# Kernel tuning notes

Hardware: AMD Instinct MI355X
Metric: run time of the kernel (lower is better)

The kernel has to match this reference:

```python
import jax, jax.numpy as jnp
import numpy as np

N, S, D = 16, 32, 256      # batch, seq_len, hidden_size
B = 4                      # sample_size (Monte-Carlo beams)
CH = 4 * D                 # cell_hidden_dim = 4*hidden (hard-coded in __init__)
EPS = 1e-20


def _ln(x, g, b):
    m = x.mean(-1, keepdims=True)
    v = ((x - m) ** 2).mean(-1, keepdims=True)
    return (x - m) / jnp.sqrt(v + 1e-5) * g + b


def _masked_softmax(logits, mask):
    p = jax.nn.softmax(logits, axis=-1)
    p = p * mask + EPS
    return p / p.sum(-1, keepdims=True)


def _cell(l, r, w1, b1, w2, b2, ln2_g, ln2_b):
    # TreeLSTM-style fused cell: Linear -> GELU -> Linear -> gates -> LayerNorm
    cat = jnp.concatenate([l, r], axis=-1)                  # (NB, s, 2D)
    inter = jax.nn.gelu(cat @ w1 + b1, approximate=False)   # (NB, s, 4D)
    contents = (inter @ w2 + b2).reshape(*l.shape[:-1], 4, D)
    gates = jax.nn.sigmoid(contents[..., 0:3, :])
    f1, f2, ig = gates[..., 0, :], gates[..., 1, :], gates[..., 2, :]
    parent = contents[..., 3, :]
    return _ln(f1 * l + f2 * r + ig * parent, ln2_g, ln2_b)


def _select(old_h, new_h, mask, accu, dec_W, dec_b, key):
    NB, Sc, Dd = new_h.shape
    old_l, old_r = old_h[:, :-1], old_h[:, 1:]
    nh = new_h * mask[:, :, None]
    pad = jnp.zeros((NB, 1, Dd), nh.dtype)
    l1 = jnp.concatenate([pad, nh[:, :-1]], axis=1)
    l2 = jnp.concatenate([pad, l1[:, :-1]], axis=1)
    r1 = jnp.concatenate([nh[:, 1:], pad], axis=1)
    r2 = jnp.concatenate([r1[:, 1:], pad], axis=1)
    win = jnp.concatenate([l2, l1, nh, r1, r2], axis=-1)    # (NB, Sc, 5D)
    logits = (win @ dec_W + dec_b)[..., 0] / np.sqrt(5 * Dd)
    # straight-through Gumbel softmax (temperature = 1)
    u = jax.random.uniform(key, logits.shape, logits.dtype)
    g = -jnp.log(-jnp.log(u + EPS) + EPS)
    y_soft = _masked_softmax(logits + g, mask)
    y_hard = jax.nn.one_hot(jnp.argmax(y_soft, axis=-1), Sc, dtype=y_soft.dtype)
    sel = jax.lax.stop_gradient(y_hard - y_soft) + y_soft
    soft_scores = jnp.sum(sel * _masked_softmax(logits, mask), axis=1)
    accu = accu + jnp.log(soft_scores + EPS)
    cs = jnp.cumsum(sel, axis=1)
    left = (1.0 - cs)[:, :, None]
    right = (cs - sel)[:, :, None]
    merged = sel[:, :, None] * new_h + left * old_l + right * old_r
    return merged, accu


def setup_inputs() -> dict:
    key = jax.random.key(0)
    ks = jax.random.split(key, 6)
    f32 = jnp.float32
    return {
        "x": jax.random.normal(ks[0], (N, S, D), f32),
        "input_mask": jnp.ones((N, S), f32),
        "word_W": jax.random.normal(ks[1], (D, D), f32) / np.sqrt(D),
        "word_b": jnp.zeros((D,), f32),
        "ln_g": jnp.ones((D,), f32),
        "ln_b": jnp.zeros((D,), f32),
        "w1": jax.random.normal(ks[2], (2 * D, CH), f32) / np.sqrt(2 * D),
        "b1": jnp.zeros((CH,), f32),
        "w2": jax.random.normal(ks[3], (CH, 4 * D), f32) / np.sqrt(CH),
        "b2": jnp.zeros((4 * D,), f32),
        "ln2_g": jnp.ones((D,), f32),
        "ln2_b": jnp.zeros((D,), f32),
        "dec_W": jax.random.normal(ks[4], (5 * D, 1), f32) / np.sqrt(5 * D),
        "dec_b": jnp.zeros((1,), f32),
    }


def reference(x, input_mask, word_W, word_b, ln_g, ln_b, w1, b1, w2, b2,
              ln2_g, ln2_b, dec_W, dec_b):
    state = _ln(x @ word_W + word_b, ln_g, ln_b)                 # (N, S, D)
    state = jnp.repeat(state[:, None], B, axis=1).reshape(N * B, S, D)
    lmask = jnp.repeat(input_mask[:, None], B, axis=1).reshape(N * B, S)
    accu = jnp.zeros((N * B,), state.dtype)
    base = jax.random.key(1234)
    # sequential tree-building recurrence; sequence axis shrinks by 1 each step
    for i in range(S - 1):
        l, r = state[:, :-1], state[:, 1:]
        new_state = _cell(l, r, w1, b1, w2, b2, ln2_g, ln2_b)
        if i < S - 2:
            new_state, new_accu = _select(state, new_state, lmask[:, i + 1:],
                                          accu, dec_W, dec_b,
                                          jax.random.fold_in(base, i))
        else:
            new_accu = accu
        done = lmask[:, i + 1]
        state = done[:, None, None] * new_state + (1.0 - done[:, None, None]) * state[:, :-1]
        accu = done * new_accu + (1.0 - done) * accu
    h = state[:, 0].reshape(N, B, D)
    scores = jax.nn.softmax(accu.reshape(N, B, 1), axis=1)
    return jnp.sum(scores * h, axis=1)                            # (N, D)
```

## Files before the change

kernel.cpp:

```cpp
#include <hip/hip_runtime.h>
#include <cstdint>
#include <cstddef>

namespace {
constexpr int kP0 = 31;
constexpr int kM0 = 496;
}

__device__ float g_state[2][64 * 32 * 256];
__device__ float g_nh[2][64 * kP0 * 256];
__device__ float g_s5[2][64 * kP0 * 5];
__device__ float g_nh0[kM0 * 256];
__device__ float g_s50[kM0 * 5];
__device__ float g_inter0[(size_t)kM0 * 1024];
__device__ float g_cont0[(size_t)kM0 * 1024];
__device__ float g_p1[4][128 * 1024];
__device__ float g_p2[4][128 * 1024];
__device__ float g_accu[64];
__device__ int g_slots[2][128];

__device__ __forceinline__ void tf2x32(uint32_t k0, uint32_t k1, uint32_t x0,
                                       uint32_t x1, uint32_t& o0, uint32_t& o1) {
  uint32_t ks2 = k0 ^ k1 ^ 0x1BD11BDAu;
  x0 += k0; x1 += k1;
#define TF_ROT(v, r) (((v) << (r)) | ((v) >> (32 - (r))))
#define TF_RD(r) { x0 += x1; x1 = TF_ROT(x1, r); x1 ^= x0; }
  TF_RD(13) TF_RD(15) TF_RD(26) TF_RD(6)   x0 += k1;  x1 += ks2 + 1u;
  TF_RD(17) TF_RD(29) TF_RD(16) TF_RD(24)  x0 += ks2; x1 += k0 + 2u;
  TF_RD(13) TF_RD(15) TF_RD(26) TF_RD(6)   x0 += k0;  x1 += k1 + 3u;
  TF_RD(17) TF_RD(29) TF_RD(16) TF_RD(24)  x0 += k1;  x1 += ks2 + 4u;
  TF_RD(13) TF_RD(15) TF_RD(26) TF_RD(6)   x0 += ks2; x1 += k0 + 5u;
  o0 = x0; o1 = x1;
#undef TF_RD
#undef TF_ROT
}

__device__ __forceinline__ float blockSum256(float v, float* red4, int tid) {
#pragma unroll
  for (int o = 32; o > 0; o >>= 1) v += __shfl_down(v, o, 64);
  __syncthreads();
  if ((tid & 63) == 0) red4[tid >> 6] = v;
  __syncthreads();
  return red4[0] + red4[1] + red4[2] + red4[3];
}
__device__ __forceinline__ float waveMax64(float v) {
#pragma unroll
  for (int o = 32; o > 0; o >>= 1) v = fmaxf(v, __shfl_xor(v, o, 64));
  return v;
}
__device__ __forceinline__ float waveSum64(float v) {
#pragma unroll
  for (int o = 32; o > 0; o >>= 1) v += __shfl_xor(v, o, 64);
  return v;
}
__device__ __forceinline__ float geluf(float v) {
  return 0.5f * v * (1.0f + erff(v * 0.70710678118654752440f));
}

__global__ __launch_bounds__(256) void k_embed(const float* __restrict__ x,
                                               const float* __restrict__ wW,
                                               const float* __restrict__ wb,
                                               const float* __restrict__ lng,
                                               const float* __restrict__ lnb) {
  int row = blockIdx.x;
  int d = threadIdx.x;
  __shared__ float xs[256];
  __shared__ float red4[4];
  xs[d] = x[row * 256 + d];
  __syncthreads();
  float acc = wb[d];
  for (int k = 0; k < 256; ++k) acc = fmaf(xs[k], wW[k * 256 + d], acc);
  float mean = blockSum256(acc, red4, d) * (1.0f / 256.0f);
  float cen = acc - mean;
  float var = blockSum256(cen * cen, red4, d) * (1.0f / 256.0f);
  float o = cen / sqrtf(var + 1e-5f) * lng[d] + lnb[d];
  int n = row >> 5, s = row & 31;
#pragma unroll
  for (int bb = 0; bb < 4; ++bb)
    g_state[0][((n * 4 + bb) * 32 + s) * 256 + d] = o;
  if (row == 0 && d < 64) g_accu[d] = 0.0f;
}


__global__ __launch_bounds__(256) void k_g1s(const float* __restrict__ w1,
                                             const float* __restrict__ b1) {
  __shared__ float As[64][17];
  __shared__ float Ws[64][68];
  const int tid = threadIdx.x;
  const int colB = blockIdx.x * 64;
  const int rowB = blockIdx.y * 16;
  const int row = tid >> 4, cg = tid & 15;
  const int ar = tid >> 4, ak = (tid & 15) * 4;
  const float* Ab;
  {
    int m = rowB + ar;
    int n = m / 31, j = m - n * 31;
    Ab = g_state[0] + (n * 4) * 8192 + j * 256;
  }
  float4 aR = *(const float4*)&Ab[ak];
  float4 wR[4];
#pragma unroll
  for (int q = 0; q < 4; ++q) {
    int f = tid + q * 256; int kk = f >> 4, c4 = f & 15;
    wR[q] = *(const float4*)&w1[(size_t)kk * 1024 + colB + c4 * 4];
  }
  float acc[4] = {};
  for (int c = 0; c < 8; ++c) {
    As[ak + 0][ar] = aR.x; As[ak + 1][ar] = aR.y;
    As[ak + 2][ar] = aR.z; As[ak + 3][ar] = aR.w;
#pragma unroll
    for (int q = 0; q < 4; ++q) {
      int f = tid + q * 256; int kk = f >> 4, c4 = f & 15;
      *(float4*)&Ws[kk][c4 * 4] = wR[q];
    }
    __syncthreads();
    if (c < 7) {
      int kb = (c + 1) * 64;
      aR = *(const float4*)&Ab[kb + ak];
#pragma unroll
      for (int q = 0; q < 4; ++q) {
        int f = tid + q * 256; int kk = f >> 4, c4 = f & 15;
        wR[q] = *(const float4*)&w1[(size_t)(kb + kk) * 1024 + colB + c4 * 4];
      }
    }
#pragma unroll
    for (int kk = 0; kk < 64; ++kk) {
      float a = As[kk][row];
      float4 w = *(const float4*)&Ws[kk][cg * 4];
      acc[0] = fmaf(a, w.x, acc[0]); acc[1] = fmaf(a, w.y, acc[1]);
      acc[2] = fmaf(a, w.z, acc[2]); acc[3] = fmaf(a, w.w, acc[3]);
    }
    __syncthreads();
  }
  int m = rowB + row;
  int col = colB + cg * 4;
  float4 bb = *(const float4*)&b1[col];
  float4 o;
  o.x = geluf(acc[0] + bb.x); o.y = geluf(acc[1] + bb.y);
  o.z = geluf(acc[2] + bb.z); o.w = geluf(acc[3] + bb.w);
  *(float4*)&g_inter0[(size_t)m * 1024 + col] = o;
}

__global__ __launch_bounds__(256) void k_g2s(const float* __restrict__ w2) {
  __shared__ float As[64][17];
  __shared__ float Ws[64][68];
  const int tid = threadIdx.x;
  const int colB = blockIdx.x * 64;
  const int rowB = blockIdx.y * 16;
  const int row = tid >> 4, cg = tid & 15;
  const int ar = tid >> 4, ak = (tid & 15) * 4;
  const float* Ab = g_inter0 + (size_t)(rowB + ar) * 1024;
  float4 aR = *(const float4*)&Ab[ak];
  float4 wR[4];
#pragma unroll
  for (int q = 0; q < 4; ++q) {
    int f = tid + q * 256; int kk = f >> 4, c4 = f & 15;
    wR[q] = *(const float4*)&w2[(size_t)kk * 1024 + colB + c4 * 4];
  }
  float acc[4] = {};
  for (int c = 0; c < 16; ++c) {
    As[ak + 0][ar] = aR.x; As[ak + 1][ar] = aR.y;
    As[ak + 2][ar] = aR.z; As[ak + 3][ar] = aR.w;
#pragma unroll
    for (int q = 0; q < 4; ++q) {
      int f = tid + q * 256; int kk = f >> 4, c4 = f & 15;
      *(float4*)&Ws[kk][c4 * 4] = wR[q];
    }
    __syncthreads();
    if (c < 15) {
      int kb = (c + 1) * 64;
      aR = *(const float4*)&Ab[kb + ak];
#pragma unroll
      for (int q = 0; q < 4; ++q) {
        int f = tid + q * 256; int kk = f >> 4, c4 = f & 15;
        wR[q] = *(const float4*)&w2[(size_t)(kb + kk) * 1024 + colB + c4 * 4];
      }
    }
#pragma unroll
    for (int kk = 0; kk < 64; ++kk) {
      float a = As[kk][row];
      float4 w = *(const float4*)&Ws[kk][cg * 4];
      acc[0] = fmaf(a, w.x, acc[0]); acc[1] = fmaf(a, w.y, acc[1]);
      acc[2] = fmaf(a, w.z, acc[2]); acc[3] = fmaf(a, w.w, acc[3]);
    }
    __syncthreads();
  }
  int m = rowB + row;
  int col = colB + cg * 4;
  float4 o = {acc[0], acc[1], acc[2], acc[3]};
  *(float4*)&g_cont0[(size_t)m * 1024 + col] = o;
}

__device__ __forceinline__ float4 g2t_loadA(int grow, int kpos, const float* __restrict__ b1) {
  size_t g = (size_t)grow * 1024 + kpos;
  float4 p0 = *(const float4*)&g_p1[0][g];
  float4 p1 = *(const float4*)&g_p1[1][g];
  float4 p2 = *(const float4*)&g_p1[2][g];
  float4 p3 = *(const float4*)&g_p1[3][g];
  float4 bb = *(const float4*)&b1[kpos];
  float4 r;
  r.x = geluf(p0.x + p1.x + p2.x + p3.x + bb.x);
  r.y = geluf(p0.y + p1.y + p2.y + p3.y + bb.y);
  r.z = geluf(p0.z + p1.z + p2.z + p3.z + bb.z);
  r.w = geluf(p0.w + p1.w + p2.w + p3.w + bb.w);
  return r;
}

__global__ __launch_bounds__(256) void k_g2t(const float* __restrict__ w2,
                                             const float* __restrict__ b1) {
  __shared__ float As[64][17];
  __shared__ float Ws[64][68];
  const int tid = threadIdx.x;
  const int colB = blockIdx.x * 64;
  const int rowB = blockIdx.y * 16;
  const int Ks = blockIdx.z;
  const int kb0 = Ks * 256;
  const int row = tid >> 4, cg = tid & 15;
  const int ar = tid >> 4, ak = (tid & 15) * 4;
  const int grow = rowB + ar;
  float4 aR = g2t_loadA(grow, kb0 + ak, b1);
  float4 wR[4];
#pragma unroll
  for (int q = 0; q < 4; ++q) {
    int f = tid + q * 256; int kk = f >> 4, c4 = f & 15;
    wR[q] = *(const float4*)&w2[(size_t)(kb0 + kk) * 1024 + colB + c4 * 4];
  }
  float acc[4] = {};
  for (int c = 0; c < 4; ++c) {
    As[ak + 0][ar] = aR.x; As[ak + 1][ar] = aR.y;
    As[ak + 2][ar] = aR.z; As[ak + 3][ar] = aR.w;
#pragma unroll
    for (int q = 0; q < 4; ++q) {
      int f = tid + q * 256; int kk = f >> 4, c4 = f & 15;
      *(float4*)&Ws[kk][c4 * 4] = wR[q];
    }
    __syncthreads();
    if (c < 3) {
      int kb = kb0 + (c + 1) * 64;
      aR = g2t_loadA(grow, kb + ak, b1);
#pragma unroll
      for (int q = 0; q < 4; ++q) {
        int f = tid + q * 256; int kk = f >> 4, c4 = f & 15;
        wR[q] = *(const float4*)&w2[(size_t)(kb + kk) * 1024 + colB + c4 * 4];
      }
    }
#pragma unroll
    for (int kk = 0; kk < 64; ++kk) {
      float a = As[kk][row];
      float4 w = *(const float4*)&Ws[kk][cg * 4];
      acc[0] = fmaf(a, w.x, acc[0]); acc[1] = fmaf(a, w.y, acc[1]);
      acc[2] = fmaf(a, w.z, acc[2]); acc[3] = fmaf(a, w.w, acc[3]);
    }
    __syncthreads();
  }
  int col = colB + cg * 4;
  float4 o = {acc[0], acc[1], acc[2], acc[3]};
  *(float4*)&g_p2[Ks][(rowB + row) * 1024 + col] = o;
}

__global__ __launch_bounds__(256) void k_cellfull(const float* __restrict__ imask,
                                                  const float* __restrict__ ln2g,
                                                  const float* __restrict__ ln2b,
                                                  const float* __restrict__ decW,
                                                  const float* __restrict__ b2) {
  int m = blockIdx.x;
  int d = threadIdx.x;
  int n = m / 31, j = m - n * 31;
  const float* st = g_state[0] + (n * 4) * 8192;
  const float* crow = g_cont0 + (size_t)m * 1024;
  float c0 = crow[d] + b2[d];
  float c1 = crow[256 + d] + b2[256 + d];
  float c2 = crow[512 + d] + b2[512 + d];
  float c3 = crow[768 + d] + b2[768 + d];
  float l = st[j * 256 + d];
  float r = st[(j + 1) * 256 + d];
  float f1 = 1.0f / (1.0f + expf(-c0));
  float f2 = 1.0f / (1.0f + expf(-c1));
  float ig = 1.0f / (1.0f + expf(-c2));
  float pre = f1 * l + f2 * r + ig * c3;
  __shared__ float red4[4];
  __shared__ float w5[4][5];
  float mean = blockSum256(pre, red4, d) * (1.0f / 256.0f);
  float cen = pre - mean;
  float var = blockSum256(cen * cen, red4, d) * (1.0f / 256.0f);
  float nh = cen / sqrtf(var + 1e-5f) * ln2g[d] + ln2b[d];
  g_nh0[m * 256 + d] = nh;
  float mv = imask[n * 32 + 1 + j];
  float nhm = nh * mv;
  float pv[5];
#pragma unroll
  for (int t = 0; t < 5; ++t) pv[t] = nhm * decW[t * 256 + d];
#pragma unroll
  for (int t = 0; t < 5; ++t)
#pragma unroll
    for (int o = 32; o > 0; o >>= 1) pv[t] += __shfl_down(pv[t], o, 64);
  __syncthreads();
  if ((d & 63) == 0) {
#pragma unroll
    for (int t = 0; t < 5; ++t) w5[d >> 6][t] = pv[t];
  }
  __syncthreads();
  if (d < 5) g_s50[m * 5 + d] = w5[0][d] + w5[1][d] + w5[2][d] + w5[3][d];
}

__global__ __launch_bounds__(256) void k_cm(
    const float* __restrict__ imask, const float* __restrict__ decW,
    const float* __restrict__ decb, const float* __restrict__ b2,
    const float* __restrict__ ln2g, const float* __restrict__ ln2b,
    const float* __restrict__ w1, int i, int last) {
  const int b = blockIdx.x, grp = blockIdx.y;
  const int tid = threadIdx.x, st = tid, lane = tid & 63, wv = tid >> 6;
  const int Sc = 31 - i;
  const int buf = i & 1;
  const int n32 = (b >> 2) * 32;
  __shared__ float sh_nhf[2][256];
  __shared__ float sh_s5f[2][5];
  __shared__ float sA[3][256];
  __shared__ float red4[4];
  __shared__ float w5s[4][5];
  __shared__ int sh_k;
  __shared__ float sh_sv;
  int slot0 = -1, slot1 = -1;
  if (i > 0) { slot0 = g_slots[buf][2 * b]; slot1 = g_slots[buf][2 * b + 1]; }
  const float* s5Src = (i == 0) ? (g_s50 + (b >> 2) * kP0 * 5) : (g_s5[buf] + b * kP0 * 5);
  const float* nhSrcG = (i == 0) ? (g_nh0 + (size_t)(b >> 2) * kP0 * 256)
                                 : (g_nh[buf] + (size_t)b * kP0 * 256);
  const float* stOld = g_state[buf] + b * 8192;
  float* stNew = g_state[(i + 1) & 1] + b * 8192;
  float* nhDst = g_nh[(i + 1) & 1] + (size_t)b * kP0 * 256;
  float* s5Dst = g_s5[(i + 1) & 1] + b * kP0 * 5;
  float done = imask[n32 + i + 1];

  if (i > 0) {
#pragma unroll 1
    for (int s = 0; s < 2; ++s) {
      int j = (s == 0) ? slot0 : slot1;
      if (j < 0) continue;
      int sr = 2 * b + s;
      float c[4];
#pragma unroll
      for (int q = 0; q < 4; ++q) {
        int g = sr * 1024 + q * 256 + st;
        float v = ((g_p2[0][g] + g_p2[1][g]) + g_p2[2][g]) + g_p2[3][g];
        c[q] = v + b2[q * 256 + st];
      }
      float l = stOld[j * 256 + st];
      float r = stOld[(j + 1) * 256 + st];
      float f1 = 1.0f / (1.0f + expf(-c[0]));
      float f2 = 1.0f / (1.0f + expf(-c[1]));
      float ig = 1.0f / (1.0f + expf(-c[2]));
      float pre = f1 * l + f2 * r + ig * c[3];
      float mean = blockSum256(pre, red4, st) * (1.0f / 256.0f);
      float cen = pre - mean;
      float var = blockSum256(cen * cen, red4, st) * (1.0f / 256.0f);
      float nh = cen / sqrtf(var + 1e-5f) * ln2g[st] + ln2b[st];
      sh_nhf[s][st] = nh;
      float mv = imask[n32 + i + 1 + j];
      float nhm = nh * mv;
      float pv[5];
#pragma unroll
      for (int t = 0; t < 5; ++t) pv[t] = nhm * decW[t * 256 + st];
#pragma unroll
      for (int t = 0; t < 5; ++t) {
        float v = pv[t];
#pragma unroll
        for (int o = 32; o > 0; o >>= 1) v += __shfl_down(v, o, 64);
        pv[t] = v;
      }
      __syncthreads();
      if (lane == 0) {
#pragma unroll
        for (int t = 0; t < 5; ++t) w5s[wv][t] = pv[t];
      }
      __syncthreads();
      if (st < 5) sh_s5f[s][st] = w5s[0][st] + w5s[1][st] + w5s[2][st] + w5s[3][st];
    }
  }
  __syncthreads();

  if (!last && tid < 64) {
    int j = lane;
    bool act = j < Sc;
    float mv = 0.f, lg = 0.f;
    if (act) {
      mv = imask[n32 + i + 1 + j];
      float t5 = decb[0];
      if (j >= 2) {
        int rw = j - 2;
        t5 += (i > 0 && rw == slot0) ? sh_s5f[0][0] : (i > 0 && rw == slot1) ? sh_s5f[1][0] : s5Src[rw * 5 + 0];
      }
      if (j >= 1) {
        int rw = j - 1;
        t5 += (i > 0 && rw == slot0) ? sh_s5f[0][1] : (i > 0 && rw == slot1) ? sh_s5f[1][1] : s5Src[rw * 5 + 1];
      }
      {
        int rw = j;
        t5 += (i > 0 && rw == slot0) ? sh_s5f[0][2] : (i > 0 && rw == slot1) ? sh_s5f[1][2] : s5Src[rw * 5 + 2];
      }
      if (j + 1 < Sc) {
        int rw = j + 1;
        t5 += (i > 0 && rw == slot0) ? sh_s5f[0][3] : (i > 0 && rw == slot1) ? sh_s5f[1][3] : s5Src[rw * 5 + 3];
      }
      if (j + 2 < Sc) {
        int rw = j + 2;
        t5 += (i > 0 && rw == slot0) ? sh_s5f[0][4] : (i > 0 && rw == slot1) ? sh_s5f[1][4] : s5Src[rw * 5 + 4];
      }
      lg = t5 / 35.77708763999664f;
    }
    uint32_t fk0, fk1, o0, o1;
    tf2x32(0u, 1234u, 0u, (uint32_t)i, fk0, fk1);
    uint32_t idx = (uint32_t)(b * Sc + j);
    tf2x32(fk0, fk1, 0u, idx, o0, o1);
    uint32_t bits = o0 ^ o1;
    float u = __uint_as_float((bits >> 9) | 0x3f800000u) - 1.0f;
    float gum = -logf(-logf(u + 1e-20f) + 1e-20f);
    float z = lg + gum;
    float zm = waveMax64(act ? z : -3.0e38f);
    float e = act ? expf(z - zm) : 0.f;
    float p = e / waveSum64(e);
    float y = act ? (p * mv + 1e-20f) : 0.f;
    float ys = y / waveSum64(y);
    float av = act ? ys : -1.f;
    int ai = j;
#pragma unroll
    for (int o = 32; o > 0; o >>= 1) {
      float ov = __shfl_xor(av, o, 64);
      int oi = __shfl_xor(ai, o, 64);
      if (ov > av || (ov == av && oi < ai)) { av = ov; ai = oi; }
    }
    float lm = waveMax64(act ? lg : -3.0e38f);
    float e2 = act ? expf(lg - lm) : 0.f;
    float p2 = e2 / waveSum64(e2);
    float y2 = act ? (p2 * mv + 1e-20f) : 0.f;
    float ps = y2 / waveSum64(y2);
    float ysk = __shfl(ys, ai, 64);
    float psk = __shfl(ps, ai, 64);
    float sv = (1.0f - ysk) + ysk;
    if (j == 0) {
      sh_k = ai;
      sh_sv = sv;
      if (grp == 0) {
        g_accu[b] += done * logf(sv * psk + 1e-20f);
        int s0 = -1, s1 = -1;
        if (done != 0.0f) {
          if (ai >= 1) s0 = ai - 1;
          if (ai <= Sc - 2) s1 = ai;
        }
        g_slots[(i + 1) & 1][2 * b] = s0;
        g_slots[(i + 1) & 1][2 * b + 1] = s1;
      }
    }
  }
  __syncthreads();

  if (last) {
    if (grp == 0 && wv == 0) {
      float4 ol = *(const float4*)&stOld[lane * 4];
      float4 nh4;
      if (slot0 == 0) nh4 = *(const float4*)&sh_nhf[0][lane * 4];
      else if (slot1 == 0) nh4 = *(const float4*)&sh_nhf[1][lane * 4];
      else nh4 = *(const float4*)&nhSrcG[lane * 4];
      float4 o4;
      o4.x = done * nh4.x + (1.0f - done) * ol.x;
      o4.y = done * nh4.y + (1.0f - done) * ol.y;
      o4.z = done * nh4.z + (1.0f - done) * ol.z;
      o4.w = done * nh4.w + (1.0f - done) * ol.w;
      *(float4*)&stNew[lane * 4] = o4;
    }
    return;
  }

  int k = sh_k;
  float sv = sh_sv;
  {
    int jrow = grp * 4 + wv;
    if (jrow < Sc) {
      float4 ol = *(const float4*)&stOld[jrow * 256 + lane * 4];
      float4 ov4;
      if (done != 0.0f) {
        float4 mg;
        if (jrow < k) {
          mg = ol;
        } else if (jrow == k) {
          float4 nh4 = (i > 0 && k == slot0) ? *(const float4*)&sh_nhf[0][lane * 4]
                     : (i > 0 && k == slot1) ? *(const float4*)&sh_nhf[1][lane * 4]
                     : *(const float4*)&nhSrcG[k * 256 + lane * 4];
          mg.x = sv * nh4.x + (1.0f - sv) * ol.x;
          mg.y = sv * nh4.y + (1.0f - sv) * ol.y;
          mg.z = sv * nh4.z + (1.0f - sv) * ol.z;
          mg.w = sv * nh4.w + (1.0f - sv) * ol.w;
        } else {
          float4 orr = *(const float4*)&stOld[(jrow + 1) * 256 + lane * 4];
          mg.x = (1.0f - sv) * ol.x + sv * orr.x;
          mg.y = (1.0f - sv) * ol.y + sv * orr.y;
          mg.z = (1.0f - sv) * ol.z + sv * orr.z;
          mg.w = (1.0f - sv) * ol.w + sv * orr.w;
        }
        ov4.x = done * mg.x + (1.0f - done) * ol.x;
        ov4.y = done * mg.y + (1.0f - done) * ol.y;
        ov4.z = done * mg.z + (1.0f - done) * ol.z;
        ov4.w = done * mg.w + (1.0f - done) * ol.w;
      } else {
        ov4 = ol;
      }
      *(float4*)&stNew[jrow * 256 + lane * 4] = ov4;
      if (jrow < Sc - 1) {
        int src = (done != 0.0f && jrow > k) ? jrow + 1 : jrow;
        float4 nv = (i > 0 && src == slot0) ? *(const float4*)&sh_nhf[0][lane * 4]
                  : (i > 0 && src == slot1) ? *(const float4*)&sh_nhf[1][lane * 4]
                  : *(const float4*)&nhSrcG[src * 256 + lane * 4];
        *(float4*)&nhDst[jrow * 256 + lane * 4] = nv;
        float mv2 = imask[n32 + i + 2 + jrow];
        float pv[5];
#pragma unroll
        for (int t = 0; t < 5; ++t) {
          const float* dw = decW + t * 256 + lane * 4;
          pv[t] = (nv.x * dw[0] + nv.y * dw[1] + nv.z * dw[2] + nv.w * dw[3]) * mv2;
        }
#pragma unroll
        for (int t = 0; t < 5; ++t) {
          float v = pv[t];
#pragma unroll
          for (int o = 32; o > 0; o >>= 1) v += __shfl_down(v, o, 64);
          pv[t] = v;
        }
        if (lane == 0) {
#pragma unroll
          for (int t = 0; t < 5; ++t) s5Dst[jrow * 5 + t] = pv[t];
        }
      }
    }
  }

  if (done != 0.0f) {
    __syncthreads();
    {
      int d = st;
      float nhKv = (i > 0 && k == slot0) ? sh_nhf[0][d]
                 : (i > 0 && k == slot1) ? sh_nhf[1][d]
                 : nhSrcG[k * 256 + d];
#pragma unroll
      for (int t = 0; t < 3; ++t) {
        int r = k - 1 + t;
        if (r < 0 || r > Sc - 1) continue;
        float ol = stOld[r * 256 + d];
        float mg;
        if (r < k) mg = ol;
        else if (r == k) mg = sv * nhKv + (1.0f - sv) * ol;
        else mg = (1.0f - sv) * ol + sv * stOld[(r + 1) * 256 + d];
        sA[t][d] = done * mg + (1.0f - done) * ol;
      }
    }
    __syncthreads();
    const int my = grp >> 2;
    const int Ks = grp & 3;
    const int has = (my == 0) ? (k >= 1) : (k <= Sc - 2);
    const int kb0 = Ks * 128;
    const float* A = (my == 0) ? ((Ks < 2) ? sA[0] : sA[1])
                               : ((Ks < 2) ? sA[1] : sA[2]);
    const int koff = (Ks < 2) ? kb0 : (kb0 - 256);
    const int col = st * 4;
    float a0 = 0.f, a1 = 0.f, a2 = 0.f, a3 = 0.f;
    for (int kk = 0; kk < 128; ++kk) {
      float4 w = *(const float4*)&w1[(size_t)(kb0 + kk) * 1024 + col];
      float av = A[koff + kk];
      a0 = fmaf(av, w.x, a0); a1 = fmaf(av, w.y, a1);
      a2 = fmaf(av, w.z, a2); a3 = fmaf(av, w.w, a3);
    }
    if (has) {
      float4 o = {a0, a1, a2, a3};
      *(float4*)&g_p1[Ks][(2 * b + my) * 1024 + col] = o;
    }
  }
}

__global__ __launch_bounds__(256) void k_final(float* __restrict__ out) {
  int n = blockIdx.x, d = threadIdx.x;
  float a0 = g_accu[n * 4 + 0], a1 = g_accu[n * 4 + 1];
  float a2 = g_accu[n * 4 + 2], a3 = g_accu[n * 4 + 3];
  float mx = fmaxf(fmaxf(a0, a1), fmaxf(a2, a3));
  float e0 = expf(a0 - mx), e1 = expf(a1 - mx), e2 = expf(a2 - mx), e3 = expf(a3 - mx);
  float ssum = e0 + e1 + e2 + e3;
  const float* st1 = g_state[1];
  float h0 = st1[(n * 4 + 0) * 8192 + d];
  float h1 = st1[(n * 4 + 1) * 8192 + d];
  float h2 = st1[(n * 4 + 2) * 8192 + d];
  float h3 = st1[(n * 4 + 3) * 8192 + d];
  out[n * 256 + d] = (e0 / ssum) * h0 + (e1 / ssum) * h1 + (e2 / ssum) * h2 + (e3 / ssum) * h3;
}

extern "C" void kernel_launch(void* const* d_in, const int* in_sizes, int n_in,
                              void* d_out, int out_size, void* d_ws, size_t ws_size,
                              hipStream_t stream) {
  (void)in_sizes; (void)n_in; (void)d_ws; (void)ws_size; (void)out_size;
  const float* x = (const float*)d_in[0];
  const float* imask = (const float*)d_in[1];
  const float* wW = (const float*)d_in[2];
  const float* wb = (const float*)d_in[3];
  const float* lng = (const float*)d_in[4];
  const float* lnb = (const float*)d_in[5];
  const float* w1 = (const float*)d_in[6];
  const float* b1 = (const float*)d_in[7];
  const float* w2 = (const float*)d_in[8];
  const float* b2 = (const float*)d_in[9];
  const float* ln2g = (const float*)d_in[10];
  const float* ln2b = (const float*)d_in[11];
  const float* decW = (const float*)d_in[12];
  const float* decb = (const float*)d_in[13];
  float* out = (float*)d_out;

  k_embed<<<dim3(512), dim3(256), 0, stream>>>(x, wW, wb, lng, lnb);
  k_g1s<<<dim3(16, 31), dim3(256), 0, stream>>>(w1, b1);
  k_g2s<<<dim3(16, 31), dim3(256), 0, stream>>>(w2);
  k_cellfull<<<dim3(kM0), dim3(256), 0, stream>>>(imask, ln2g, ln2b, decW, b2);
  k_cm<<<dim3(64, 8), dim3(256), 0, stream>>>(imask, decW, decb, b2, ln2g, ln2b, w1, 0, 0);
  for (int i = 1; i <= 30; ++i) {
    k_g2t<<<dim3(16, 8, 4), dim3(256), 0, stream>>>(w2, b1);
    int lastf = (i == 30) ? 1 : 0;
    k_cm<<<dim3(64, lastf ? 1 : 8), dim3(256), 0, stream>>>(imask, decW, decb, b2,
                                                            ln2g, ln2b, w1, i, lastf);
  }
  k_final<<<dim3(16), dim3(256), 0, stream>>>(out);
}
```

Measured before the change: 1.248 ms.

## Use 4x4 register tiles in GEMMs and halve k_cm grid with dual-row accumulation

The three SGEMM kernels move from one output row per thread to a 4x4 register micro-tile with 128-thread blocks and wider column or row tiles. The register double-buffered prefetch is dropped for direct global-to-shared loads. In k_cm each thread now computes both neighbour rows against one w1 load, and handles two state rows per warp, which halves the grid's y dimension. The aim is more FMAs per shared or global load and half the w1 traffic in the recurrent step, at the cost of fewer blocks (less parallelism) and no load/compute overlap.

```diff
diff --git a/kernel.cpp b/kernel.cpp
--- a/kernel.cpp
+++ b/kernel.cpp
@@ -82,113 +82,113 @@
 }
 
 
-__global__ __launch_bounds__(256) void k_g1s(const float* __restrict__ w1,
+__global__ __launch_bounds__(128) void k_g1s(const float* __restrict__ w1,
                                              const float* __restrict__ b1) {
-  __shared__ float As[64][17];
-  __shared__ float Ws[64][68];
+  __shared__ float As[64][20];
+  __shared__ float Ws[64][132];
   const int tid = threadIdx.x;
-  const int colB = blockIdx.x * 64;
+  const int colB = blockIdx.x * 128;
   const int rowB = blockIdx.y * 16;
-  const int row = tid >> 4, cg = tid & 15;
-  const int ar = tid >> 4, ak = (tid & 15) * 4;
+  const int rg = tid >> 5, cgp = tid & 31;
+  const int ar = tid & 15, kq = tid >> 4;
+  const int wc = tid & 31, wk = tid >> 5;
   const float* Ab;
   {
     int m = rowB + ar;
     int n = m / 31, j = m - n * 31;
     Ab = g_state[0] + (n * 4) * 8192 + j * 256;
   }
-  float4 aR = *(const float4*)&Ab[ak];
-  float4 wR[4];
-#pragma unroll
-  for (int q = 0; q < 4; ++q) {
-    int f = tid + q * 256; int kk = f >> 4, c4 = f & 15;
-    wR[q] = *(const float4*)&w1[(size_t)kk * 1024 + colB + c4 * 4];
-  }
-  float acc[4] = {};
+  float acc[4][4] = {};
   for (int c = 0; c < 8; ++c) {
-    As[ak + 0][ar] = aR.x; As[ak + 1][ar] = aR.y;
-    As[ak + 2][ar] = aR.z; As[ak + 3][ar] = aR.w;
-#pragma unroll
-    for (int q = 0; q < 4; ++q) {
-      int f = tid + q * 256; int kk = f >> 4, c4 = f & 15;
-      *(float4*)&Ws[kk][c4 * 4] = wR[q];
-    }
-    __syncthreads();
-    if (c < 7) {
-      int kb = (c + 1) * 64;
-      aR = *(const float4*)&Ab[kb + ak];
-#pragma unroll
-      for (int q = 0; q < 4; ++q) {
-        int f = tid + q * 256; int kk = f >> 4, c4 = f & 15;
-        wR[q] = *(const float4*)&w1[(size_t)(kb + kk) * 1024 + colB + c4 * 4];
-      }
-    }
+    const int kb = c * 64;
+#pragma unroll
+    for (int q = 0; q < 2; ++q) {
+      int kp = kq * 8 + q * 4;
+      float4 a = *(const float4*)&Ab[kb + kp];
+      As[kp + 0][ar] = a.x; As[kp + 1][ar] = a.y;
+      As[kp + 2][ar] = a.z; As[kp + 3][ar] = a.w;
+    }
+#pragma unroll
+    for (int q = 0; q < 16; ++q) {
+      int kk = wk * 16 + q;
+      *(float4*)&Ws[kk][wc * 4] =
+          *(const float4*)&w1[(size_t)(kb + kk) * 1024 + colB + wc * 4];
+    }
+    __syncthreads();
 #pragma unroll
     for (int kk = 0; kk < 64; ++kk) {
-      float a = As[kk][row];
-      float4 w = *(const float4*)&Ws[kk][cg * 4];
-      acc[0] = fmaf(a, w.x, acc[0]); acc[1] = fmaf(a, w.y, acc[1]);
-      acc[2] = fmaf(a, w.z, acc[2]); acc[3] = fmaf(a, w.w, acc[3]);
-    }
-    __syncthreads();
-  }
-  int m = rowB + row;
-  int col = colB + cg * 4;
+      float4 a4 = *(const float4*)&As[kk][rg * 4];
+      float4 w4 = *(const float4*)&Ws[kk][cgp * 4];
+      float av[4] = {a4.x, a4.y, a4.z, a4.w};
+      float wv[4] = {w4.x, w4.y, w4.z, w4.w};
+#pragma unroll
+      for (int ri = 0; ri < 4; ++ri)
+#pragma unroll
+        for (int ci = 0; ci < 4; ++ci)
+          acc[ri][ci] = fmaf(av[ri], wv[ci], acc[ri][ci]);
+    }
+    __syncthreads();
+  }
+  const int col = colB + cgp * 4;
   float4 bb = *(const float4*)&b1[col];
-  float4 o;
-  o.x = geluf(acc[0] + bb.x); o.y = geluf(acc[1] + bb.y);
-  o.z = geluf(acc[2] + bb.z); o.w = geluf(acc[3] + bb.w);
-  *(float4*)&g_inter0[(size_t)m * 1024 + col] = o;
-}
-
-__global__ __launch_bounds__(256) void k_g2s(const float* __restrict__ w2) {
-  __shared__ float As[64][17];
-  __shared__ float Ws[64][68];
+#pragma unroll
+  for (int ri = 0; ri < 4; ++ri) {
+    int m = rowB + rg * 4 + ri;
+    float4 o;
+    o.x = geluf(acc[ri][0] + bb.x); o.y = geluf(acc[ri][1] + bb.y);
+    o.z = geluf(acc[ri][2] + bb.z); o.w = geluf(acc[ri][3] + bb.w);
+    *(float4*)&g_inter0[(size_t)m * 1024 + col] = o;
+  }
+}
+
+__global__ __launch_bounds__(128) void k_g2s(const float* __restrict__ w2) {
+  __shared__ float As[64][20];
+  __shared__ float Ws[64][132];
   const int tid = threadIdx.x;
-  const int colB = blockIdx.x * 64;
+  const int colB = blockIdx.x * 128;
   const int rowB = blockIdx.y * 16;
-  const int row = tid >> 4, cg = tid & 15;
-  const int ar = tid >> 4, ak = (tid & 15) * 4;
+  const int rg = tid >> 5, cgp = tid & 31;
+  const int ar = tid & 15, kq = tid >> 4;
+  const int wc = tid & 31, wk = tid >> 5;
   const float* Ab = g_inter0 + (size_t)(rowB + ar) * 1024;
-  float4 aR = *(const float4*)&Ab[ak];
-  float4 wR[4];
-#pragma unroll
-  for (int q = 0; q < 4; ++q) {
-    int f = tid + q * 256; int kk = f >> 4, c4 = f & 15;
-    wR[q] = *(const float4*)&w2[(size_t)kk * 1024 + colB + c4 * 4];
-  }
-  float acc[4] = {};
+  float acc[4][4] = {};
   for (int c = 0; c < 16; ++c) {
-    As[ak + 0][ar] = aR.x; As[ak + 1][ar] = aR.y;
-    As[ak + 2][ar] = aR.z; As[ak + 3][ar] = aR.w;
-#pragma unroll
-    for (int q = 0; q < 4; ++q) {
-      int f = tid + q * 256; int kk = f >> 4, c4 = f & 15;
-      *(float4*)&Ws[kk][c4 * 4] = wR[q];
-    }
-    __syncthreads();
-    if (c < 15) {
-      int kb = (c + 1) * 64;
-      aR = *(const float4*)&Ab[kb + ak];
-#pragma unroll
-      for (int q = 0; q < 4; ++q) {
-        int f = tid + q * 256; int kk = f >> 4, c4 = f & 15;
-        wR[q] = *(const float4*)&w2[(size_t)(kb + kk) * 1024 + colB + c4 * 4];
-      }
-    }
+    const int kb = c * 64;
+#pragma unroll
+    for (int q = 0; q < 2; ++q) {
+      int kp = kq * 8 + q * 4;
+      float4 a = *(const float4*)&Ab[kb + kp];
+      As[kp + 0][ar] = a.x; As[kp + 1][ar] = a.y;
+      As[kp + 2][ar] = a.z; As[kp + 3][ar] = a.w;
+    }
+#pragma unroll
+    for (int q = 0; q < 16; ++q) {
+      int kk = wk * 16 + q;
+      *(float4*)&Ws[kk][wc * 4] =
+          *(const float4*)&w2[(size_t)(kb + kk) * 1024 + colB + wc * 4];
+    }
+    __syncthreads();
 #pragma unroll
     for (int kk = 0; kk < 64; ++kk) {
-      float a = As[kk][row];
-      float4 w = *(const float4*)&Ws[kk][cg * 4];
-      acc[0] = fmaf(a, w.x, acc[0]); acc[1] = fmaf(a, w.y, acc[1]);
-      acc[2] = fmaf(a, w.z, acc[2]); acc[3] = fmaf(a, w.w, acc[3]);
-    }
-    __syncthreads();
-  }
-  int m = rowB + row;
-  int col = colB + cg * 4;
-  float4 o = {acc[0], acc[1], acc[2], acc[3]};
-  *(float4*)&g_cont0[(size_t)m * 1024 + col] = o;
+      float4 a4 = *(const float4*)&As[kk][rg * 4];
+      float4 w4 = *(const float4*)&Ws[kk][cgp * 4];
+      float av[4] = {a4.x, a4.y, a4.z, a4.w};
+      float wv[4] = {w4.x, w4.y, w4.z, w4.w};
+#pragma unroll
+      for (int ri = 0; ri < 4; ++ri)
+#pragma unroll
+        for (int ci = 0; ci < 4; ++ci)
+          acc[ri][ci] = fmaf(av[ri], wv[ci], acc[ri][ci]);
+    }
+    __syncthreads();
+  }
+  const int col = colB + cgp * 4;
+#pragma unroll
+  for (int ri = 0; ri < 4; ++ri) {
+    int m = rowB + rg * 4 + ri;
+    float4 o = {acc[ri][0], acc[ri][1], acc[ri][2], acc[ri][3]};
+    *(float4*)&g_cont0[(size_t)m * 1024 + col] = o;
+  }
 }
 
 __device__ __forceinline__ float4 g2t_loadA(int grow, int kpos, const float* __restrict__ b1) {
@@ -206,56 +206,57 @@
   return r;
 }
 
-__global__ __launch_bounds__(256) void k_g2t(const float* __restrict__ w2,
+__global__ __launch_bounds__(128) void k_g2t(const float* __restrict__ w2,
                                              const float* __restrict__ b1) {
-  __shared__ float As[64][17];
+  __shared__ float As[64][36];
   __shared__ float Ws[64][68];
   const int tid = threadIdx.x;
   const int colB = blockIdx.x * 64;
-  const int rowB = blockIdx.y * 16;
+  const int rowB = blockIdx.y * 32;
   const int Ks = blockIdx.z;
   const int kb0 = Ks * 256;
-  const int row = tid >> 4, cg = tid & 15;
-  const int ar = tid >> 4, ak = (tid & 15) * 4;
+  const int rg = tid >> 4, cgp = tid & 15;
+  const int ar = tid & 31, kq = tid >> 5;
+  const int wc = tid & 15, wk = tid >> 4;
   const int grow = rowB + ar;
-  float4 aR = g2t_loadA(grow, kb0 + ak, b1);
-  float4 wR[4];
-#pragma unroll
-  for (int q = 0; q < 4; ++q) {
-    int f = tid + q * 256; int kk = f >> 4, c4 = f & 15;
-    wR[q] = *(const float4*)&w2[(size_t)(kb0 + kk) * 1024 + colB + c4 * 4];
-  }
-  float acc[4] = {};
+  float acc[4][4] = {};
   for (int c = 0; c < 4; ++c) {
-    As[ak + 0][ar] = aR.x; As[ak + 1][ar] = aR.y;
-    As[ak + 2][ar] = aR.z; As[ak + 3][ar] = aR.w;
+    const int kb = kb0 + c * 64;
 #pragma unroll
     for (int q = 0; q < 4; ++q) {
-      int f = tid + q * 256; int kk = f >> 4, c4 = f & 15;
-      *(float4*)&Ws[kk][c4 * 4] = wR[q];
-    }
-    __syncthreads();
-    if (c < 3) {
-      int kb = kb0 + (c + 1) * 64;
-      aR = g2t_loadA(grow, kb + ak, b1);
-#pragma unroll
-      for (int q = 0; q < 4; ++q) {
-        int f = tid + q * 256; int kk = f >> 4, c4 = f & 15;
-        wR[q] = *(const float4*)&w2[(size_t)(kb + kk) * 1024 + colB + c4 * 4];
-      }
-    }
+      int kp = kq * 16 + q * 4;
+      float4 a = g2t_loadA(grow, kb + kp, b1);
+      As[kp + 0][ar] = a.x; As[kp + 1][ar] = a.y;
+      As[kp + 2][ar] = a.z; As[kp + 3][ar] = a.w;
+    }
+#pragma unroll
+    for (int q = 0; q < 8; ++q) {
+      int kk = wk * 8 + q;
+      *(float4*)&Ws[kk][wc * 4] =
+          *(const float4*)&w2[(size_t)(kb + kk) * 1024 + colB + wc * 4];
+    }
+    __syncthreads();
 #pragma unroll
     for (int kk = 0; kk < 64; ++kk) {
-      float a = As[kk][row];
-      float4 w = *(const float4*)&Ws[kk][cg * 4];
-      acc[0] = fmaf(a, w.x, acc[0]); acc[1] = fmaf(a, w.y, acc[1]);
-      acc[2] = fmaf(a, w.z, acc[2]); acc[3] = fmaf(a, w.w, acc[3]);
-    }
-    __syncthreads();
-  }
-  int col = colB + cg * 4;
-  float4 o = {acc[0], acc[1], acc[2], acc[3]};
-  *(float4*)&g_p2[Ks][(rowB + row) * 1024 + col] = o;
+      float4 a4 = *(const float4*)&As[kk][rg * 4];
+      float4 w4 = *(const float4*)&Ws[kk][cgp * 4];
+      float av[4] = {a4.x, a4.y, a4.z, a4.w};
+      float wv[4] = {w4.x, w4.y, w4.z, w4.w};
+#pragma unroll
+      for (int ri = 0; ri < 4; ++ri)
+#pragma unroll
+        for (int ci = 0; ci < 4; ++ci)
+          acc[ri][ci] = fmaf(av[ri], wv[ci], acc[ri][ci]);
+    }
+    __syncthreads();
+  }
+  const int col = colB + cgp * 4;
+#pragma unroll
+  for (int ri = 0; ri < 4; ++ri) {
+    int r = rowB + rg * 4 + ri;
+    float4 o = {acc[ri][0], acc[ri][1], acc[ri][2], acc[ri][3]};
+    *(float4*)&g_p2[Ks][r * 1024 + col] = o;
+  }
 }
 
 __global__ __launch_bounds__(256) void k_cellfull(const float* __restrict__ imask,
@@ -472,62 +473,62 @@
 
   int k = sh_k;
   float sv = sh_sv;
-  {
-    int jrow = grp * 4 + wv;
-    if (jrow < Sc) {
-      float4 ol = *(const float4*)&stOld[jrow * 256 + lane * 4];
-      float4 ov4;
-      if (done != 0.0f) {
-        float4 mg;
-        if (jrow < k) {
-          mg = ol;
-        } else if (jrow == k) {
-          float4 nh4 = (i > 0 && k == slot0) ? *(const float4*)&sh_nhf[0][lane * 4]
-                     : (i > 0 && k == slot1) ? *(const float4*)&sh_nhf[1][lane * 4]
-                     : *(const float4*)&nhSrcG[k * 256 + lane * 4];
-          mg.x = sv * nh4.x + (1.0f - sv) * ol.x;
-          mg.y = sv * nh4.y + (1.0f - sv) * ol.y;
-          mg.z = sv * nh4.z + (1.0f - sv) * ol.z;
-          mg.w = sv * nh4.w + (1.0f - sv) * ol.w;
-        } else {
-          float4 orr = *(const float4*)&stOld[(jrow + 1) * 256 + lane * 4];
-          mg.x = (1.0f - sv) * ol.x + sv * orr.x;
-          mg.y = (1.0f - sv) * ol.y + sv * orr.y;
-          mg.z = (1.0f - sv) * ol.z + sv * orr.z;
-          mg.w = (1.0f - sv) * ol.w + sv * orr.w;
-        }
-        ov4.x = done * mg.x + (1.0f - done) * ol.x;
-        ov4.y = done * mg.y + (1.0f - done) * ol.y;
-        ov4.z = done * mg.z + (1.0f - done) * ol.z;
-        ov4.w = done * mg.w + (1.0f - done) * ol.w;
+#pragma unroll 1
+  for (int rr = 0; rr < 2; ++rr) {
+    int jrow = grp * 8 + wv * 2 + rr;
+    if (jrow >= Sc) continue;
+    float4 ol = *(const float4*)&stOld[jrow * 256 + lane * 4];
+    float4 ov4;
+    if (done != 0.0f) {
+      float4 mg;
+      if (jrow < k) {
+        mg = ol;
+      } else if (jrow == k) {
+        float4 nh4 = (i > 0 && k == slot0) ? *(const float4*)&sh_nhf[0][lane * 4]
+                   : (i > 0 && k == slot1) ? *(const float4*)&sh_nhf[1][lane * 4]
+                   : *(const float4*)&nhSrcG[k * 256 + lane * 4];
+        mg.x = sv * nh4.x + (1.0f - sv) * ol.x;
+        mg.y = sv * nh4.y + (1.0f - sv) * ol.y;
+        mg.z = sv * nh4.z + (1.0f - sv) * ol.z;
+        mg.w = sv * nh4.w + (1.0f - sv) * ol.w;
       } else {
-        ov4 = ol;
-      }
-      *(float4*)&stNew[jrow * 256 + lane * 4] = ov4;
-      if (jrow < Sc - 1) {
-        int src = (done != 0.0f && jrow > k) ? jrow + 1 : jrow;
-        float4 nv = (i > 0 && src == slot0) ? *(const float4*)&sh_nhf[0][lane * 4]
-                  : (i > 0 && src == slot1) ? *(const float4*)&sh_nhf[1][lane * 4]
-                  : *(const float4*)&nhSrcG[src * 256 + lane * 4];
-        *(float4*)&nhDst[jrow * 256 + lane * 4] = nv;
-        float mv2 = imask[n32 + i + 2 + jrow];
-        float pv[5];
-#pragma unroll
-        for (int t = 0; t < 5; ++t) {
-          const float* dw = decW + t * 256 + lane * 4;
-          pv[t] = (nv.x * dw[0] + nv.y * dw[1] + nv.z * dw[2] + nv.w * dw[3]) * mv2;
-        }
-#pragma unroll
-        for (int t = 0; t < 5; ++t) {
-          float v = pv[t];
-#pragma unroll
-          for (int o = 32; o > 0; o >>= 1) v += __shfl_down(v, o, 64);
-          pv[t] = v;
-        }
-        if (lane == 0) {
-#pragma unroll
-          for (int t = 0; t < 5; ++t) s5Dst[jrow * 5 + t] = pv[t];
-        }
+        float4 orr = *(const float4*)&stOld[(jrow + 1) * 256 + lane * 4];
+        mg.x = (1.0f - sv) * ol.x + sv * orr.x;
+        mg.y = (1.0f - sv) * ol.y + sv * orr.y;
+        mg.z = (1.0f - sv) * ol.z + sv * orr.z;
+        mg.w = (1.0f - sv) * ol.w + sv * orr.w;
+      }
+      ov4.x = done * mg.x + (1.0f - done) * ol.x;
+      ov4.y = done * mg.y + (1.0f - done) * ol.y;
+      ov4.z = done * mg.z + (1.0f - done) * ol.z;
+      ov4.w = done * mg.w + (1.0f - done) * ol.w;
+    } else {
+      ov4 = ol;
+    }
+    *(float4*)&stNew[jrow * 256 + lane * 4] = ov4;
+    if (jrow < Sc - 1) {
+      int src = (done != 0.0f && jrow > k) ? jrow + 1 : jrow;
+      float4 nv = (i > 0 && src == slot0) ? *(const float4*)&sh_nhf[0][lane * 4]
+                : (i > 0 && src == slot1) ? *(const float4*)&sh_nhf[1][lane * 4]
+                : *(const float4*)&nhSrcG[src * 256 + lane * 4];
+      *(float4*)&nhDst[jrow * 256 + lane * 4] = nv;
+      float mv2 = imask[n32 + i + 2 + jrow];
+      float pv[5];
+#pragma unroll
+      for (int t = 0; t < 5; ++t) {
+        const float* dw = decW + t * 256 + lane * 4;
+        pv[t] = (nv.x * dw[0] + nv.y * dw[1] + nv.z * dw[2] + nv.w * dw[3]) * mv2;
+      }
+#pragma unroll
+      for (int t = 0; t < 5; ++t) {
+        float v = pv[t];
+#pragma unroll
+        for (int o = 32; o > 0; o >>= 1) v += __shfl_down(v, o, 64);
+        pv[t] = v;
+      }
+      if (lane == 0) {
+#pragma unroll
+        for (int t = 0; t < 5; ++t) s5Dst[jrow * 5 + t] = pv[t];
       }
     }
   }
@@ -552,24 +553,32 @@
       }
     }
     __syncthreads();
-    const int my = grp >> 2;
-    const int Ks = grp & 3;
-    const int has = (my == 0) ? (k >= 1) : (k <= Sc - 2);
+    const int Ks = grp;
+    const int has0 = (k >= 1);
+    const int has1 = (k <= Sc - 2);
     const int kb0 = Ks * 128;
-    const float* A = (my == 0) ? ((Ks < 2) ? sA[0] : sA[1])
-                               : ((Ks < 2) ? sA[1] : sA[2]);
+    const float* A0 = (Ks < 2) ? sA[0] : sA[1];
+    const float* A1 = (Ks < 2) ? sA[1] : sA[2];
     const int koff = (Ks < 2) ? kb0 : (kb0 - 256);
     const int col = st * 4;
-    float a0 = 0.f, a1 = 0.f, a2 = 0.f, a3 = 0.f;
+    float a00 = 0.f, a01 = 0.f, a02 = 0.f, a03 = 0.f;
+    float a10 = 0.f, a11 = 0.f, a12 = 0.f, a13 = 0.f;
     for (int kk = 0; kk < 128; ++kk) {
       float4 w = *(const float4*)&w1[(size_t)(kb0 + kk) * 1024 + col];
-      float av = A[koff + kk];
-      a0 = fmaf(av, w.x, a0); a1 = fmaf(av, w.y, a1);
-      a2 = fmaf(av, w.z, a2); a3 = fmaf(av, w.w, a3);
-    }
-    if (has) {
-      float4 o = {a0, a1, a2, a3};
-      *(float4*)&g_p1[Ks][(2 * b + my) * 1024 + col] = o;
+      float av0 = A0[koff + kk];
+      float av1 = A1[koff + kk];
+      a00 = fmaf(av0, w.x, a00); a01 = fmaf(av0, w.y, a01);
+      a02 = fmaf(av0, w.z, a02); a03 = fmaf(av0, w.w, a03);
+      a10 = fmaf(av1, w.x, a10); a11 = fmaf(av1, w.y, a11);
+      a12 = fmaf(av1, w.z, a12); a13 = fmaf(av1, w.w, a13);
+    }
+    if (has0) {
+      float4 o = {a00, a01, a02, a03};
+      *(float4*)&g_p1[Ks][(2 * b + 0) * 1024 + col] = o;
+    }
+    if (has1) {
+      float4 o = {a10, a11, a12, a13};
+      *(float4*)&g_p1[Ks][(2 * b + 1) * 1024 + col] = o;
     }
   }
 }
@@ -610,14 +619,14 @@
   float* out = (float*)d_out;
 
   k_embed<<<dim3(512), dim3(256), 0, stream>>>(x, wW, wb, lng, lnb);
-  k_g1s<<<dim3(16, 31), dim3(256), 0, stream>>>(w1, b1);
-  k_g2s<<<dim3(16, 31), dim3(256), 0, stream>>>(w2);
+  k_g1s<<<dim3(8, 31), dim3(128), 0, stream>>>(w1, b1);
+  k_g2s<<<dim3(8, 31), dim3(128), 0, stream>>>(w2);
   k_cellfull<<<dim3(kM0), dim3(256), 0, stream>>>(imask, ln2g, ln2b, decW, b2);
-  k_cm<<<dim3(64, 8), dim3(256), 0, stream>>>(imask, decW, decb, b2, ln2g, ln2b, w1, 0, 0);
+  k_cm<<<dim3(64, 4), dim3(256), 0, stream>>>(imask, decW, decb, b2, ln2g, ln2b, w1, 0, 0);
   for (int i = 1; i <= 30; ++i) {
-    k_g2t<<<dim3(16, 8, 4), dim3(256), 0, stream>>>(w2, b1);
+    k_g2t<<<dim3(16, 4, 4), dim3(128), 0, stream>>>(w2, b1);
     int lastf = (i == 30) ? 1 : 0;
-    k_cm<<<dim3(64, lastf ? 1 : 8), dim3(256), 0, stream>>>(imask, decW, decb, b2,
+    k_cm<<<dim3(64, lastf ? 1 : 4), dim3(256), 0, stream>>>(imask, decW, decb, b2,
                                                             ln2g, ln2b, w1, i, lastf);
   }
   k_final<<<dim3(16), dim3(256), 0, stream>>>(out);
```

Measured after the change: 1.324 ms. +6.1%, slower.
